# Kernel tuning notes

Hardware: AMD Instinct MI355X
Metric: run time of the kernel (lower is better)

The kernel has to match this reference:

```python
import jax, jax.numpy as jnp
import numpy as np
import math

EMBED_DIM = 1024
NUM_HEADS = 16
HEAD_DIM = EMBED_DIM // NUM_HEADS


def alibi_slopes(num_heads: int) -> np.ndarray:
    def slopes_pow2(n):
        start = 2.0 ** (-(2.0 ** (-(math.log2(n) - 3))))
        return [start * (start ** i) for i in range(n)]
    if math.log2(num_heads).is_integer():
        return np.array(slopes_pow2(num_heads), dtype=np.float32)
    closest = 2 ** math.floor(math.log2(num_heads))
    extra = slopes_pow2(2 * closest)[closest:]
    return np.array(slopes_pow2(closest) + extra[: num_heads - closest], dtype=np.float32)


def setup_inputs() -> dict:
    key = jax.random.key(0)
    ks = jax.random.split(key, 9)
    B, S, E = 2, 2048, EMBED_DIM
    scale = 1.0 / math.sqrt(E)
    x = jax.random.normal(ks[0], (B, S, E), dtype=jnp.float32)
    Wq = jax.random.normal(ks[1], (E, E), dtype=jnp.float32) * scale
    Wk = jax.random.normal(ks[2], (E, E), dtype=jnp.float32) * scale
    Wv = jax.random.normal(ks[3], (E, E), dtype=jnp.float32) * scale
    Wo = jax.random.normal(ks[4], (E, E), dtype=jnp.float32) * scale
    bq = jax.random.normal(ks[5], (E,), dtype=jnp.float32) * 0.01
    bk = jax.random.normal(ks[6], (E,), dtype=jnp.float32) * 0.01
    bv = jax.random.normal(ks[7], (E,), dtype=jnp.float32) * 0.01
    bo = jax.random.normal(ks[8], (E,), dtype=jnp.float32) * 0.01
    return {"x": x, "Wq": Wq, "bq": bq, "Wk": Wk, "bk": bk,
            "Wv": Wv, "bv": bv, "Wo": Wo, "bo": bo}


def reference(x, Wq, bq, Wk, bk, Wv, bv, Wo, bo):
    B, S, E = x.shape
    H, D = NUM_HEADS, HEAD_DIM
    # Linear layers (torch convention: y = x @ W.T + b)
    q = (x @ Wq.T + bq).reshape(B, S, H, D).transpose(0, 2, 1, 3)  # [B,H,S,D]
    k = (x @ Wk.T + bk).reshape(B, S, H, D).transpose(0, 2, 1, 3)
    v = (x @ Wv.T + bv).reshape(B, S, H, D).transpose(0, 2, 1, 3)

    # ALiBi bias: -slope_h * |i - j|
    slopes = jnp.asarray(alibi_slopes(H))                      # [H]
    pos = jnp.arange(S, dtype=jnp.float32)
    rel = jnp.abs(pos[None, :] - pos[:, None])                 # [S,S]
    bias = -slopes[:, None, None] * rel[None, :, :]            # [H,S,S]

    scores = jnp.einsum('bhqd,bhkd->bhqk', q, k) / math.sqrt(D)
    scores = scores + bias[None]
    causal = jnp.tril(jnp.ones((S, S), dtype=bool))            # keep lower triangle
    scores = jnp.where(causal[None, None], scores, -jnp.inf)
    probs = jax.nn.softmax(scores, axis=-1)
    out = jnp.einsum('bhqk,bhkd->bhqd', probs, v)              # [B,H,S,D]
    out = out.transpose(0, 2, 1, 3).reshape(B, S, E)
    return out @ Wo.T + bo
```

## Files before the change

kernel.cpp:

```cpp
#include <hip/hip_runtime.h>
#include <hip/hip_bf16.h>

typedef __bf16 bf16;
typedef __bf16 bf16x4 __attribute__((ext_vector_type(4)));
typedef __bf16 bf16x8 __attribute__((ext_vector_type(8)));
typedef float  f32x4  __attribute__((ext_vector_type(4)));

#define NEG_BIG (-1e30f)
#define LOG2E 1.44269504088896340736f

#define AS1(p) ((const __attribute__((address_space(1))) void*)(p))
#define AS3(p) ((__attribute__((address_space(3))) void*)(p))

__device__ __forceinline__ void stage16(const void* g, void* lds_uniform_base) {
    __builtin_amdgcn_global_load_lds(AS1(g), AS3(lds_uniform_base), 16, 0, 0);
}

__device__ __forceinline__ bf16x8 cvt8(const float* __restrict__ p) {
    bf16x8 r;
#pragma unroll
    for (int i = 0; i < 8; ++i) r[i] = (bf16)p[i];
    return r;
}

template <int CTRL>
__device__ __forceinline__ float dpp_max_step(float x) {
    int v = __builtin_bit_cast(int, x);
    int s = __builtin_amdgcn_update_dpp(v, v, CTRL, 0xF, 0xF, true);
    return fmaxf(x, __builtin_bit_cast(float, s));
}
template <int CTRL>
__device__ __forceinline__ float dpp_add_step(float x) {
    int v = __builtin_bit_cast(int, x);
    int s = __builtin_amdgcn_update_dpp(v, v, CTRL, 0xF, 0xF, true);
    return x + __builtin_bit_cast(float, s);
}
__device__ __forceinline__ float red16_max(float x) {
    x = dpp_max_step<0xB1>(x);
    x = dpp_max_step<0x4E>(x);
    x = dpp_max_step<0x141>(x);
    x = dpp_max_step<0x140>(x);
    return x;
}
__device__ __forceinline__ float red16_sum(float x) {
    x = dpp_add_step<0xB1>(x);
    x = dpp_add_step<0x4E>(x);
    x = dpp_add_step<0x141>(x);
    x = dpp_add_step<0x140>(x);
    return x;
}

#if __has_builtin(__builtin_amdgcn_exp2f)
#define EXP2F(x) __builtin_amdgcn_exp2f(x)
#else
#define EXP2F(x) exp2f(x)
#endif

__global__ __launch_bounds__(256) void conv_all(
    const float* __restrict__ x,  const float* __restrict__ wq,
    const float* __restrict__ wk, const float* __restrict__ wv,
    bf16* __restrict__ xb, bf16* __restrict__ wb)
{
    const int blk = blockIdx.x;
    const float* src; bf16* dst; size_t off;
    if (blk < 2048)      { src = x;  dst = xb;           off = (size_t)blk * 2048; }
    else if (blk < 2560) { src = wq; dst = wb;           off = (size_t)(blk - 2048) * 2048; }
    else if (blk < 3072) { src = wk; dst = wb + 1048576; off = (size_t)(blk - 2560) * 2048; }
    else                 { src = wv; dst = wb + 2097152; off = (size_t)(blk - 3072) * 2048; }
    const size_t i = off + (size_t)threadIdx.x * 8;
    *(bf16x8*)(dst + i) = cvt8(src + i);
}

__global__ __launch_bounds__(256) void qkv_gemm(
    const bf16* __restrict__ Xb, const bf16* __restrict__ Wb,
    const float* __restrict__ bq, const float* __restrict__ bk, const float* __restrict__ bv,
    bf16* __restrict__ qo, bf16* __restrict__ ko, bf16* __restrict__ vo)
{
    __shared__ alignas(16) bf16 As[128 * 32];
    __shared__ alignas(16) bf16 Bs[128 * 32];

    const int t    = threadIdx.x;
    const int lane = t & 63, w = t >> 6;
    const int quad = lane >> 4, col = lane & 15;
    const int nt = blockIdx.x;
    const int mt = blockIdx.y;
    const int region = nt >> 3;
    const int n0 = (nt & 7) * 128;
    const int m0 = mt * 128;
    const int K  = 1024;

    const bf16*  W    = Wb + (size_t)region * 1048576;
    const float* bias = region == 0 ? bq : (region == 1 ? bk : bv);

    const int wm = (w >> 1) * 64, wn = (w & 1) * 64;
    f32x4 acc[4][4] = {};

    for (int k0 = 0; k0 < K; k0 += 32) {
        __syncthreads();
#pragma unroll
        for (int i = 0; i < 2; ++i) {
            int c = i * 256 + t;
            stage16(Xb + (size_t)(m0 + (c >> 2)) * K + k0 + (c & 3) * 8,
                    As + (i * 256 + w * 64) * 8);
        }
#pragma unroll
        for (int i = 0; i < 2; ++i) {
            int c = i * 256 + t;
            stage16(W + (size_t)(n0 + (c >> 2)) * K + k0 + (c & 3) * 8,
                    Bs + (i * 256 + w * 64) * 8);
        }
        __syncthreads();

        bf16x8 a[4], b[4];
#pragma unroll
        for (int i = 0; i < 4; ++i)
            a[i] = *(const bf16x8*)(As + (wm + i * 16 + col) * 32 + quad * 8);
#pragma unroll
        for (int j = 0; j < 4; ++j)
            b[j] = *(const bf16x8*)(Bs + (wn + j * 16 + col) * 32 + quad * 8);
#pragma unroll
        for (int i = 0; i < 4; ++i)
#pragma unroll
            for (int j = 0; j < 4; ++j)
                acc[i][j] = __builtin_amdgcn_mfma_f32_16x16x32_bf16(a[i], b[j], acc[i][j], 0, 0, 0);
    }

    if (region == 2) {
#pragma unroll
        for (int i = 0; i < 4; ++i) {
            const int mbase = m0 + wm + i * 16 + quad * 4;
            const int b_ = mbase >> 11, s = mbase & 2047;
#pragma unroll
            for (int j = 0; j < 4; ++j) {
                const int n = n0 + wn + j * 16 + col;
                const float bb = bias[n];
                const int h = n >> 6, d = n & 63;
                bf16x4 pk;
#pragma unroll
                for (int r = 0; r < 4; ++r) pk[r] = (bf16)(acc[i][j][r] + bb);
                *(bf16x4*)(vo + ((size_t)(b_ * 16 + h) * 64 + d) * 2048 + s) = pk;
            }
        }
    } else {
        bf16* out = region == 0 ? qo : ko;
        const float scale = region == 0 ? (0.125f * LOG2E) : 1.0f;
#pragma unroll
        for (int i = 0; i < 4; ++i) {
            const int mbase = m0 + wm + i * 16 + quad * 4;
#pragma unroll
            for (int j = 0; j < 4; ++j) {
                const int n = n0 + wn + j * 16 + col;
                const float bb = bias[n];
                const int h = n >> 6, d = n & 63;
#pragma unroll
                for (int r = 0; r < 4; ++r) {
                    const int m  = mbase + r;
                    const int b_ = m >> 11, s = m & 2047;
                    out[(((size_t)(b_ * 16 + h)) * 2048 + s) * 64 + d] =
                        (bf16)((acc[i][j][r] + bb) * scale);
                }
            }
        }
    }
}

__global__ __launch_bounds__(256) void attn_kernel(
    const bf16* __restrict__ Q, const bf16* __restrict__ Kg,
    const bf16* __restrict__ Vt, bf16* __restrict__ O)
{
    const int t    = threadIdx.x;
    const int lane = t & 63, w = t >> 6;
    const int quad = lane >> 4, col = lane & 15;
    const int bh   = blockIdx.x & 31;
    const int pair = blockIdx.x >> 5;
    const int b  = bh >> 4, h = bh & 15;
    const float nslope = -EXP2F(-0.5f * (float)(h + 1)) * LOG2E;

    const bf16* qp  = Q  + (size_t)bh * 2048 * 64;
    const bf16* kp  = Kg + (size_t)bh * 2048 * 64;
    const bf16* vtp = Vt + (size_t)bh * 64 * 2048;

    __shared__ alignas(16) bf16 Kbuf[2][128 * 64];
    __shared__ alignas(16) bf16 Vbuf[2][64 * 128];
    __shared__ alignas(16) bf16 Ps[4 * 32 * 136];
    bf16* Pw = Ps + w * (32 * 136);

    for (int pass = 0; pass < 2; ++pass) {
        const int qt = pass == 0 ? (15 - pair) : pair;
        const int q0 = qt * 128;

        bf16x8 qa[2][2];
#pragma unroll
        for (int mi = 0; mi < 2; ++mi)
#pragma unroll
            for (int ks = 0; ks < 2; ++ks)
                qa[mi][ks] = *(const bf16x8*)(qp + (size_t)(q0 + w * 32 + mi * 16 + col) * 64
                                              + ks * 32 + quad * 8);

        float mrow[2][4], lrow[2][4];
        f32x4 of[2][4] = {};
        float bi[2][4];
        int   gi0[2];
#pragma unroll
        for (int mi = 0; mi < 2; ++mi) {
            gi0[mi] = q0 + w * 32 + mi * 16 + quad * 4;
#pragma unroll
            for (int r = 0; r < 4; ++r) {
                mrow[mi][r] = NEG_BIG; lrow[mi][r] = 0.f;
                bi[mi][r] = nslope * (float)(gi0[mi] + r);
            }
        }

        {
#pragma unroll
            for (int i = 0; i < 4; ++i) {
                int c = i * 256 + t;
                int row = c >> 3, j8 = (c & 7) ^ (row & 7);
                stage16(kp + (size_t)row * 64 + j8 * 8, Kbuf[0] + (i * 256 + w * 64) * 8);
            }
#pragma unroll
            for (int i = 0; i < 4; ++i) {
                int c = i * 256 + t;
                int d = c >> 4, j8 = (c & 15) ^ (d & 7);
                stage16(vtp + (size_t)d * 2048 + j8 * 8, Vbuf[0] + (i * 256 + w * 64) * 8);
            }
        }
        __syncthreads();

        for (int kvt = 0; kvt <= qt; ++kvt) {
            const int kv0 = kvt * 128;
            const bf16* Kb = Kbuf[kvt & 1];
            const bf16* Vb = Vbuf[kvt & 1];

            if (kvt < qt) {
                bf16* Kn = Kbuf[(kvt & 1) ^ 1];
                bf16* Vn = Vbuf[(kvt & 1) ^ 1];
                const int nv0 = kv0 + 128;
#pragma unroll
                for (int i = 0; i < 4; ++i) {
                    int c = i * 256 + t;
                    int row = c >> 3, j8 = (c & 7) ^ (row & 7);
                    stage16(kp + (size_t)(nv0 + row) * 64 + j8 * 8, Kn + (i * 256 + w * 64) * 8);
                }
#pragma unroll
                for (int i = 0; i < 4; ++i) {
                    int c = i * 256 + t;
                    int d = c >> 4, j8 = (c & 15) ^ (d & 7);
                    stage16(vtp + (size_t)d * 2048 + nv0 + j8 * 8, Vn + (i * 256 + w * 64) * 8);
                }
            }

            f32x4 sc[2][8];
#pragma unroll
            for (int nj = 0; nj < 8; ++nj) {
                const int row = nj * 16 + col;
                const bf16* kb = Kb + row * 64;
                const int rx = row & 7;
                bf16x8 k0f = *(const bf16x8*)(kb + (quad ^ rx) * 8);
                bf16x8 k1f = *(const bf16x8*)(kb + ((quad + 4) ^ rx) * 8);
#pragma unroll
                for (int mi = 0; mi < 2; ++mi) {
                    f32x4 z = {};
                    z = __builtin_amdgcn_mfma_f32_16x16x32_bf16(qa[mi][0], k0f, z, 0, 0, 0);
                    z = __builtin_amdgcn_mfma_f32_16x16x32_bf16(qa[mi][1], k1f, z, 0, 0, 0);
                    sc[mi][nj] = z;
                }
            }

            const bool diag = (kvt == qt);
            float bj[8];
#pragma unroll
            for (int nj = 0; nj < 8; ++nj)
                bj[nj] = nslope * (float)(kv0 + nj * 16 + col);

#pragma unroll
            for (int mi = 0; mi < 2; ++mi) {
#pragma unroll
                for (int r = 0; r < 4; ++r) {
#pragma unroll
                    for (int nj = 0; nj < 8; ++nj)
                        sc[mi][nj][r] += bi[mi][r] - bj[nj];
                    if (diag) {
                        const int gi = gi0[mi] + r;
#pragma unroll
                        for (int nj = 0; nj < 8; ++nj)
                            if (kv0 + nj * 16 + col > gi) sc[mi][nj][r] = NEG_BIG;
                    }
                    float mx = sc[mi][0][r];
#pragma unroll
                    for (int nj = 1; nj < 8; ++nj) mx = fmaxf(mx, sc[mi][nj][r]);
                    mx = red16_max(mx);
                    const float mo = mrow[mi][r];
                    const float mn = fmaxf(mo, mx);
                    const float alpha = EXP2F(mo - mn);
                    float rs = 0.f;
#pragma unroll
                    for (int nj = 0; nj < 8; ++nj) {
                        float p = EXP2F(sc[mi][nj][r] - mn);
                        sc[mi][nj][r] = p;
                        rs += p;
                    }
                    rs = red16_sum(rs);
                    mrow[mi][r] = mn;
                    lrow[mi][r] = lrow[mi][r] * alpha + rs;
#pragma unroll
                    for (int jd = 0; jd < 4; ++jd) of[mi][jd][r] *= alpha;
                }
            }

#pragma unroll
            for (int mi = 0; mi < 2; ++mi)
#pragma unroll
                for (int nj = 0; nj < 8; ++nj)
#pragma unroll
                    for (int r = 0; r < 4; ++r)
                        Pw[(mi * 16 + quad * 4 + r) * 136 + nj * 16 + col] = (bf16)sc[mi][nj][r];

#pragma unroll
            for (int kk = 0; kk < 4; ++kk) {
                bf16x8 pa0 = *(const bf16x8*)(Pw + (col)      * 136 + kk * 32 + quad * 8);
                bf16x8 pa1 = *(const bf16x8*)(Pw + (16 + col) * 136 + kk * 32 + quad * 8);
#pragma unroll
                for (int jd = 0; jd < 4; ++jd) {
                    const int rd = jd * 16 + col;
                    bf16x8 vbf = *(const bf16x8*)(Vb + rd * 128 + (((kk * 4 + quad) ^ (rd & 7)) * 8));
                    of[0][jd] = __builtin_amdgcn_mfma_f32_16x16x32_bf16(pa0, vbf, of[0][jd], 0, 0, 0);
                    of[1][jd] = __builtin_amdgcn_mfma_f32_16x16x32_bf16(pa1, vbf, of[1][jd], 0, 0, 0);
                }
            }

            __syncthreads();
        }

#pragma unroll
        for (int mi = 0; mi < 2; ++mi)
#pragma unroll
            for (int r = 0; r < 4; ++r) {
                const int s = q0 + w * 32 + mi * 16 + quad * 4 + r;
                const float inv_l = 1.f / lrow[mi][r];
#pragma unroll
                for (int jd = 0; jd < 4; ++jd) {
                    const int e = h * 64 + jd * 16 + col;
                    O[((size_t)(b * 2048 + s)) * 1024 + e] = (bf16)(of[mi][jd][r] * inv_l);
                }
            }
    }
}

__global__ __launch_bounds__(256) void out_gemm(
    const bf16* __restrict__ A, const float* __restrict__ W,
    const float* __restrict__ bias, float* __restrict__ out)
{
    __shared__ alignas(16) bf16 As[128 * 32];
    __shared__ alignas(16) bf16 Bs[128 * 32];

    const int t    = threadIdx.x;
    const int lane = t & 63, w = t >> 6;
    const int quad = lane >> 4, col = lane & 15;
    const int n0 = blockIdx.x * 128;
    const int m0 = blockIdx.y * 128;
    const int K  = 1024;
    const int wm = (w >> 1) * 64, wn = (w & 1) * 64;
    const int r0 = t >> 2, c8 = (t & 3) * 8;
    f32x4 acc[4][4] = {};

    for (int k0 = 0; k0 < K; k0 += 32) {
        bf16x8 bx0 = cvt8(W + (size_t)(n0 + r0)      * K + k0 + c8);
        bf16x8 bx1 = cvt8(W + (size_t)(n0 + 64 + r0) * K + k0 + c8);
        __syncthreads();
#pragma unroll
        for (int i = 0; i < 2; ++i) {
            int c = i * 256 + t;
            stage16(A + (size_t)(m0 + (c >> 2)) * K + k0 + (c & 3) * 8,
                    As + (i * 256 + w * 64) * 8);
        }
        *(bf16x8*)(Bs + r0 * 32 + c8)        = bx0;
        *(bf16x8*)(Bs + (64 + r0) * 32 + c8) = bx1;
        __syncthreads();

        bf16x8 a[4], b[4];
#pragma unroll
        for (int i = 0; i < 4; ++i)
            a[i] = *(const bf16x8*)(As + (wm + i * 16 + col) * 32 + quad * 8);
#pragma unroll
        for (int j = 0; j < 4; ++j)
            b[j] = *(const bf16x8*)(Bs + (wn + j * 16 + col) * 32 + quad * 8);
#pragma unroll
        for (int i = 0; i < 4; ++i)
#pragma unroll
            for (int j = 0; j < 4; ++j)
                acc[i][j] = __builtin_amdgcn_mfma_f32_16x16x32_bf16(a[i], b[j], acc[i][j], 0, 0, 0);
    }

#pragma unroll
    for (int i = 0; i < 4; ++i) {
        const int mbase = m0 + wm + i * 16 + quad * 4;
#pragma unroll
        for (int j = 0; j < 4; ++j) {
            const int n = n0 + wn + j * 16 + col;
            const float bb = bias[n];
#pragma unroll
            for (int r = 0; r < 4; ++r)
                out[(size_t)(mbase + r) * 1024 + n] = acc[i][j][r] + bb;
        }
    }
}

extern "C" void kernel_launch(void* const* d_in, const int* in_sizes, int n_in,
                              void* d_out, int out_size, void* d_ws, size_t ws_size,
                              hipStream_t stream) {
    const float* x  = (const float*)d_in[0];
    const float* Wq = (const float*)d_in[1];
    const float* bq = (const float*)d_in[2];
    const float* Wk = (const float*)d_in[3];
    const float* bk = (const float*)d_in[4];
    const float* Wv = (const float*)d_in[5];
    const float* bv = (const float*)d_in[6];
    const float* Wo = (const float*)d_in[7];
    const float* bo = (const float*)d_in[8];
    float* out = (float*)d_out;

    bf16* xb  = (bf16*)d_ws;
    bf16* qws = xb  + 4194304;
    bf16* kws = qws + 4194304;
    bf16* vws = kws + 4194304;
    bf16* aws = xb;

    bf16* wb = (bf16*)d_out;

    conv_all<<<dim3(3584), 256, 0, stream>>>(x, Wq, Wk, Wv, xb, wb);
    qkv_gemm<<<dim3(24, 32), 256, 0, stream>>>(xb, wb, bq, bk, bv, qws, kws, vws);
    attn_kernel<<<dim3(256), 256, 0, stream>>>(qws, kws, vws, aws);
    out_gemm<<<dim3(8, 32), 256, 0, stream>>>(aws, Wo, bo, out);
}
```

Measured before the change: 216.9 us.

## Use eight waves per attention block with 16 query rows each

After: 210.7 us. -2.9%, faster.

```diff
diff --git a/kernel.cpp b/kernel.cpp
--- a/kernel.cpp
+++ b/kernel.cpp
@@ -164,7 +164,7 @@
     }
 }
 
-__global__ __launch_bounds__(256) void attn_kernel(
+__global__ __launch_bounds__(512) void attn_kernel(
     const bf16* __restrict__ Q, const bf16* __restrict__ Kg,
     const bf16* __restrict__ Vt, bf16* __restrict__ O)
 {
@@ -182,47 +182,40 @@
 
     __shared__ alignas(16) bf16 Kbuf[2][128 * 64];
     __shared__ alignas(16) bf16 Vbuf[2][64 * 128];
-    __shared__ alignas(16) bf16 Ps[4 * 32 * 136];
-    bf16* Pw = Ps + w * (32 * 136);
+    __shared__ alignas(16) bf16 Ps[8 * 16 * 136];
+    bf16* Pw = Ps + w * (16 * 136);
 
     for (int pass = 0; pass < 2; ++pass) {
         const int qt = pass == 0 ? (15 - pair) : pair;
         const int q0 = qt * 128;
 
-        bf16x8 qa[2][2];
-#pragma unroll
-        for (int mi = 0; mi < 2; ++mi)
-#pragma unroll
-            for (int ks = 0; ks < 2; ++ks)
-                qa[mi][ks] = *(const bf16x8*)(qp + (size_t)(q0 + w * 32 + mi * 16 + col) * 64
-                                              + ks * 32 + quad * 8);
-
-        float mrow[2][4], lrow[2][4];
-        f32x4 of[2][4] = {};
-        float bi[2][4];
-        int   gi0[2];
-#pragma unroll
-        for (int mi = 0; mi < 2; ++mi) {
-            gi0[mi] = q0 + w * 32 + mi * 16 + quad * 4;
-#pragma unroll
-            for (int r = 0; r < 4; ++r) {
-                mrow[mi][r] = NEG_BIG; lrow[mi][r] = 0.f;
-                bi[mi][r] = nslope * (float)(gi0[mi] + r);
-            }
+        bf16x8 qa[2];
+#pragma unroll
+        for (int ks = 0; ks < 2; ++ks)
+            qa[ks] = *(const bf16x8*)(qp + (size_t)(q0 + w * 16 + col) * 64
+                                      + ks * 32 + quad * 8);
+
+        float mrow[4], lrow[4], bi[4];
+        f32x4 of[4] = {};
+        const int gi0 = q0 + w * 16 + quad * 4;
+#pragma unroll
+        for (int r = 0; r < 4; ++r) {
+            mrow[r] = NEG_BIG; lrow[r] = 0.f;
+            bi[r] = nslope * (float)(gi0 + r);
         }
 
         {
 #pragma unroll
-            for (int i = 0; i < 4; ++i) {
-                int c = i * 256 + t;
+            for (int i = 0; i < 2; ++i) {
+                int c = i * 512 + t;
                 int row = c >> 3, j8 = (c & 7) ^ (row & 7);
-                stage16(kp + (size_t)row * 64 + j8 * 8, Kbuf[0] + (i * 256 + w * 64) * 8);
-            }
-#pragma unroll
-            for (int i = 0; i < 4; ++i) {
-                int c = i * 256 + t;
+                stage16(kp + (size_t)row * 64 + j8 * 8, Kbuf[0] + (i * 512 + w * 64) * 8);
+            }
+#pragma unroll
+            for (int i = 0; i < 2; ++i) {
+                int c = i * 512 + t;
                 int d = c >> 4, j8 = (c & 15) ^ (d & 7);
-                stage16(vtp + (size_t)d * 2048 + j8 * 8, Vbuf[0] + (i * 256 + w * 64) * 8);
+                stage16(vtp + (size_t)d * 2048 + j8 * 8, Vbuf[0] + (i * 512 + w * 64) * 8);
             }
         }
         __syncthreads();
@@ -237,20 +230,20 @@
                 bf16* Vn = Vbuf[(kvt & 1) ^ 1];
                 const int nv0 = kv0 + 128;
 #pragma unroll
-                for (int i = 0; i < 4; ++i) {
-                    int c = i * 256 + t;
+                for (int i = 0; i < 2; ++i) {
+                    int c = i * 512 + t;
                     int row = c >> 3, j8 = (c & 7) ^ (row & 7);
-                    stage16(kp + (size_t)(nv0 + row) * 64 + j8 * 8, Kn + (i * 256 + w * 64) * 8);
-                }
-#pragma unroll
-                for (int i = 0; i < 4; ++i) {
-                    int c = i * 256 + t;
+                    stage16(kp + (size_t)(nv0 + row) * 64 + j8 * 8, Kn + (i * 512 + w * 64) * 8);
+                }
+#pragma unroll
+                for (int i = 0; i < 2; ++i) {
+                    int c = i * 512 + t;
                     int d = c >> 4, j8 = (c & 15) ^ (d & 7);
-                    stage16(vtp + (size_t)d * 2048 + nv0 + j8 * 8, Vn + (i * 256 + w * 64) * 8);
-                }
-            }
-
-            f32x4 sc[2][8];
+                    stage16(vtp + (size_t)d * 2048 + nv0 + j8 * 8, Vn + (i * 512 + w * 64) * 8);
+                }
+            }
+
+            f32x4 sc[8];
 #pragma unroll
             for (int nj = 0; nj < 8; ++nj) {
                 const int row = nj * 16 + col;
@@ -258,13 +251,10 @@
                 const int rx = row & 7;
                 bf16x8 k0f = *(const bf16x8*)(kb + (quad ^ rx) * 8);
                 bf16x8 k1f = *(const bf16x8*)(kb + ((quad + 4) ^ rx) * 8);
-#pragma unroll
-                for (int mi = 0; mi < 2; ++mi) {
-                    f32x4 z = {};
-                    z = __builtin_amdgcn_mfma_f32_16x16x32_bf16(qa[mi][0], k0f, z, 0, 0, 0);
-                    z = __builtin_amdgcn_mfma_f32_16x16x32_bf16(qa[mi][1], k1f, z, 0, 0, 0);
-                    sc[mi][nj] = z;
-                }
+                f32x4 z = {};
+                z = __builtin_amdgcn_mfma_f32_16x16x32_bf16(qa[0], k0f, z, 0, 0, 0);
+                z = __builtin_amdgcn_mfma_f32_16x16x32_bf16(qa[1], k1f, z, 0, 0, 0);
+                sc[nj] = z;
             }
 
             const bool diag = (kvt == qt);
@@ -274,58 +264,51 @@
                 bj[nj] = nslope * (float)(kv0 + nj * 16 + col);
 
 #pragma unroll
-            for (int mi = 0; mi < 2; ++mi) {
-#pragma unroll
-                for (int r = 0; r < 4; ++r) {
+            for (int r = 0; r < 4; ++r) {
+#pragma unroll
+                for (int nj = 0; nj < 8; ++nj)
+                    sc[nj][r] += bi[r] - bj[nj];
+                if (diag) {
+                    const int gi = gi0 + r;
 #pragma unroll
                     for (int nj = 0; nj < 8; ++nj)
-                        sc[mi][nj][r] += bi[mi][r] - bj[nj];
-                    if (diag) {
-                        const int gi = gi0[mi] + r;
-#pragma unroll
-                        for (int nj = 0; nj < 8; ++nj)
-                            if (kv0 + nj * 16 + col > gi) sc[mi][nj][r] = NEG_BIG;
-                    }
-                    float mx = sc[mi][0][r];
-#pragma unroll
-                    for (int nj = 1; nj < 8; ++nj) mx = fmaxf(mx, sc[mi][nj][r]);
-                    mx = red16_max(mx);
-                    const float mo = mrow[mi][r];
-                    const float mn = fmaxf(mo, mx);
-                    const float alpha = EXP2F(mo - mn);
-                    float rs = 0.f;
-#pragma unroll
-                    for (int nj = 0; nj < 8; ++nj) {
-                        float p = EXP2F(sc[mi][nj][r] - mn);
-                        sc[mi][nj][r] = p;
-                        rs += p;
-                    }
-                    rs = red16_sum(rs);
-                    mrow[mi][r] = mn;
-                    lrow[mi][r] = lrow[mi][r] * alpha + rs;
-#pragma unroll
-                    for (int jd = 0; jd < 4; ++jd) of[mi][jd][r] *= alpha;
-                }
-            }
-
-#pragma unroll
-            for (int mi = 0; mi < 2; ++mi)
-#pragma unroll
-                for (int nj = 0; nj < 8; ++nj)
-#pragma unroll
-                    for (int r = 0; r < 4; ++r)
-                        Pw[(mi * 16 + quad * 4 + r) * 136 + nj * 16 + col] = (bf16)sc[mi][nj][r];
+                        if (kv0 + nj * 16 + col > gi) sc[nj][r] = NEG_BIG;
+                }
+                float mx = sc[0][r];
+#pragma unroll
+                for (int nj = 1; nj < 8; ++nj) mx = fmaxf(mx, sc[nj][r]);
+                mx = red16_max(mx);
+                const float mo = mrow[r];
+                const float mn = fmaxf(mo, mx);
+                const float alpha = EXP2F(mo - mn);
+                float rs = 0.f;
+#pragma unroll
+                for (int nj = 0; nj < 8; ++nj) {
+                    float p = EXP2F(sc[nj][r] - mn);
+                    sc[nj][r] = p;
+                    rs += p;
+                }
+                rs = red16_sum(rs);
+                mrow[r] = mn;
+                lrow[r] = lrow[r] * alpha + rs;
+#pragma unroll
+                for (int jd = 0; jd < 4; ++jd) of[jd][r] *= alpha;
+            }
+
+#pragma unroll
+            for (int nj = 0; nj < 8; ++nj)
+#pragma unroll
+                for (int r = 0; r < 4; ++r)
+                    Pw[(quad * 4 + r) * 136 + nj * 16 + col] = (bf16)sc[nj][r];
 
 #pragma unroll
             for (int kk = 0; kk < 4; ++kk) {
-                bf16x8 pa0 = *(const bf16x8*)(Pw + (col)      * 136 + kk * 32 + quad * 8);
-                bf16x8 pa1 = *(const bf16x8*)(Pw + (16 + col) * 136 + kk * 32 + quad * 8);
+                bf16x8 pa = *(const bf16x8*)(Pw + col * 136 + kk * 32 + quad * 8);
 #pragma unroll
                 for (int jd = 0; jd < 4; ++jd) {
                     const int rd = jd * 16 + col;
                     bf16x8 vbf = *(const bf16x8*)(Vb + rd * 128 + (((kk * 4 + quad) ^ (rd & 7)) * 8));
-                    of[0][jd] = __builtin_amdgcn_mfma_f32_16x16x32_bf16(pa0, vbf, of[0][jd], 0, 0, 0);
-                    of[1][jd] = __builtin_amdgcn_mfma_f32_16x16x32_bf16(pa1, vbf, of[1][jd], 0, 0, 0);
+                    of[jd] = __builtin_amdgcn_mfma_f32_16x16x32_bf16(pa, vbf, of[jd], 0, 0, 0);
                 }
             }
 
@@ -333,17 +316,15 @@
         }
 
 #pragma unroll
-        for (int mi = 0; mi < 2; ++mi)
-#pragma unroll
-            for (int r = 0; r < 4; ++r) {
-                const int s = q0 + w * 32 + mi * 16 + quad * 4 + r;
-                const float inv_l = 1.f / lrow[mi][r];
-#pragma unroll
-                for (int jd = 0; jd < 4; ++jd) {
-                    const int e = h * 64 + jd * 16 + col;
-                    O[((size_t)(b * 2048 + s)) * 1024 + e] = (bf16)(of[mi][jd][r] * inv_l);
-                }
-            }
+        for (int r = 0; r < 4; ++r) {
+            const int s = q0 + w * 16 + quad * 4 + r;
+            const float inv_l = 1.f / lrow[r];
+#pragma unroll
+            for (int jd = 0; jd < 4; ++jd) {
+                const int e = h * 64 + jd * 16 + col;
+                O[((size_t)(b * 2048 + s)) * 1024 + e] = (bf16)(of[jd][r] * inv_l);
+            }
+        }
     }
 }
 
@@ -430,6 +411,6 @@
 
     conv_all<<<dim3(3584), 256, 0, stream>>>(x, Wq, Wk, Wv, xb, wb);
     qkv_gemm<<<dim3(24, 32), 256, 0, stream>>>(xb, wb, bq, bk, bv, qws, kws, vws);
-    attn_kernel<<<dim3(256), 256, 0, stream>>>(qws, kws, vws, aws);
+    attn_kernel<<<dim3(256), 512, 0, stream>>>(qws, kws, vws, aws);
     out_gemm<<<dim3(8, 32), 256, 0, stream>>>(aws, Wo, bo, out);
 }
```
